# Optimization experiments

Hardware: AMD Instinct MI355X
Metric: run time of the kernel (lower is better)

The kernel has to match this reference:

```python
import jax, jax.numpy as jnp
import numpy as np

B, S, HID = 2, 2048, 1024
H, KVH = 16, 4           # query heads, kv heads
D = HID // H             # head_dim = 64
G = H // KVH             # group size (n_rep) = 4


def setup_inputs() -> dict:
    key = jax.random.key(0)
    ks = jax.random.split(key, 6)
    x = jax.random.normal(ks[0], (B, S, HID), dtype=jnp.float32)
    # RoPE tables: [S, D], standard theta=10000
    inv_freq = 1.0 / (10000.0 ** (jnp.arange(0, D, 2, dtype=jnp.float32) / D))
    freqs = jnp.arange(S, dtype=jnp.float32)[:, None] * inv_freq[None, :]  # [S, D/2]
    emb = jnp.concatenate([freqs, freqs], axis=-1)  # [S, D]
    cos, sin = jnp.cos(emb), jnp.sin(emb)
    scale = 0.02
    wq = jax.random.normal(ks[1], (HID, H * D), dtype=jnp.float32) * scale
    wk = jax.random.normal(ks[2], (HID, KVH * D), dtype=jnp.float32) * scale
    wv = jax.random.normal(ks[3], (HID, KVH * D), dtype=jnp.float32) * scale
    wo = jax.random.normal(ks[4], (H * D, HID), dtype=jnp.float32) * scale
    return {"x": x, "cos": cos, "sin": sin, "wq": wq, "wk": wk, "wv": wv, "wo": wo}


def _rotate_half(t):
    h = t.shape[-1] // 2
    return jnp.concatenate([-t[..., h:], t[..., :h]], axis=-1)


def reference(x, cos, sin, wq, wk, wv, wo):
    b, s, _ = x.shape
    q = (x @ wq).reshape(b, s, H, D)
    k = (x @ wk).reshape(b, s, KVH, D)
    v = (x @ wv).reshape(b, s, KVH, D)
    # RoPE (cos/sin broadcast over heads, unsqueeze_dim=1 -> [S,1,D])
    c = cos[:s, None, :]
    sn = sin[:s, None, :]
    q = q * c + _rotate_half(q) * sn
    k = k * c + _rotate_half(k) * sn
    # GQA attention without materializing repeated K/V: group q heads by kv head
    qg = q.reshape(b, s, KVH, G, D)
    scores = jnp.einsum('bqkgd,bskd->bkgqs', qg, k) / jnp.sqrt(jnp.asarray(D, q.dtype))
    causal = jnp.tril(jnp.ones((s, s), dtype=bool))  # [S_q, S_k]
    scores = jnp.where(causal[None, None, None, :, :], scores, -jnp.inf)
    p = jax.nn.softmax(scores, axis=-1)
    out = jnp.einsum('bkgqs,bskd->bqkgd', p, v).reshape(b, s, H * D)
    return out @ wo
```

## Files before the change

### kernel.cpp

```cpp
#include <hip/hip_runtime.h>
#include <hip/hip_bf16.h>


typedef short bfx4 __attribute__((ext_vector_type(4)));
typedef short bfx8 __attribute__((ext_vector_type(8)));
typedef float fx4  __attribute__((ext_vector_type(4)));
typedef float fx16 __attribute__((ext_vector_type(16)));
typedef unsigned int ux4 __attribute__((ext_vector_type(4)));

#define DEV __device__ __forceinline__
#define ALPHA 0.18033688011112042f

DEV void load_lds16(const void* g, void* l) {
  __builtin_amdgcn_global_load_lds(
      (const __attribute__((address_space(1))) unsigned int*)g,
      (__attribute__((address_space(3))) unsigned int*)l, 16, 0, 0);
}

DEV unsigned short f2bf(float f) {
  unsigned int x = __builtin_bit_cast(unsigned int, f);
  unsigned int r = (x + 0x7fffu + ((x >> 16) & 1u)) >> 16;
  return (unsigned short)r;
}
DEV float exp2_fast(float x) { float r; asm("v_exp_f32 %0, %1" : "=v"(r) : "v"(x)); return r; }
DEV unsigned cvtpk(float lo, float hi) {
  unsigned r; asm("v_cvt_pk_bf16_f32 %0, %1, %2" : "=v"(r) : "v"(lo), "v"(hi)); return r;
}
#define MFMA32 __builtin_amdgcn_mfma_f32_32x32x16_bf16


__global__ __launch_bounds__(256) void cvt_x_kernel(const float* __restrict__ x,
                                                    unsigned short* __restrict__ out) {
  int i = (blockIdx.x * 256 + threadIdx.x) * 8;
  fx4 a = *(const fx4*)(x + i);
  fx4 b = *(const fx4*)(x + i + 4);
  bfx8 r;
  r[0] = (short)f2bf(a[0]); r[1] = (short)f2bf(a[1]);
  r[2] = (short)f2bf(a[2]); r[3] = (short)f2bf(a[3]);
  r[4] = (short)f2bf(b[0]); r[5] = (short)f2bf(b[1]);
  r[6] = (short)f2bf(b[2]); r[7] = (short)f2bf(b[3]);
  *(bfx8*)(out + i) = r;
}


__global__ __launch_bounds__(256) void tw_kernel(const float* __restrict__ wq,
                                                 const float* __restrict__ wk,
                                                 const float* __restrict__ wv,
                                                 const float* __restrict__ wo,
                                                 unsigned short* __restrict__ wqkvT,
                                                 unsigned short* __restrict__ woT) {
  __shared__ float tile[64 * 65];
  const int bx = blockIdx.x;
  const int c0 = blockIdx.y * 64;
  const float* src; int ncols, rofs, r0; unsigned short* dst;
  if (bx < 24) {
    r0 = bx * 64; dst = wqkvT;
    if (r0 < 1024)      { src = wq; ncols = 1024; rofs = r0; }
    else if (r0 < 1280) { src = wk; ncols = 256;  rofs = r0 - 1024; }
    else                { src = wv; ncols = 256;  rofs = r0 - 1280; }
  } else {
    r0 = (bx - 24) * 64; dst = woT; src = wo; ncols = 1024; rofs = r0;
  }
  const int t = threadIdx.x;
#pragma unroll
  for (int p = 0; p < 4; ++p) {
    int idx = p * 256 + t;
    int cc = idx >> 4, q4 = idx & 15;
    fx4 v = *(const fx4*)(src + (size_t)(c0 + cc) * ncols + rofs + q4 * 4);
#pragma unroll
    for (int i = 0; i < 4; ++i) tile[(q4 * 4 + i) * 65 + cc] = v[i];
  }
  __syncthreads();
#pragma unroll
  for (int p = 0; p < 2; ++p) {
    int idx = p * 256 + t;
    int rr = idx >> 3, c8 = idx & 7;
    bfx8 v8;
#pragma unroll
    for (int i = 0; i < 8; ++i) v8[i] = (short)f2bf(tile[rr * 65 + c8 * 8 + i]);
    *(bfx8*)(dst + (size_t)(r0 + rr) * 1024 + c0 + c8 * 8) = v8;
  }
}


template <bool OUT_BF16, bool FUSE_ROPE>
__global__ __launch_bounds__(256) void gemm_bt_kernel(const unsigned short* __restrict__ A,
                                                      const unsigned short* __restrict__ Bt,
                                                      void* __restrict__ Cp,
                                                      int K, int ldc,
                                                      const float* __restrict__ ct,
                                                      const float* __restrict__ st,
                                                      unsigned short* __restrict__ vTout) {
  __shared__ __align__(16) unsigned short As[64 * 32];
  __shared__ __align__(16) unsigned short Bs[128 * 32];
  const int t = threadIdx.x;
  const int l = t & 63;
  const int w = t >> 6;
  const int wm = (w >> 1) * 32, wn = (w & 1) * 64;
  const int bm = blockIdx.x, bn = blockIdx.y;
  fx4 acc[2][4] = {};

  for (int kt = 0; kt < K; kt += 32) {
    __syncthreads();
    {
      int rr = t >> 2, ca = t & 3;
      int gca = ((ca ^ ((rr >> 1) & 3)) * 8);
      load_lds16(A + (size_t)(bm * 64 + rr) * K + kt + gca, (char*)As + t * 16);
    }
#pragma unroll
    for (int p = 0; p < 2; ++p) {
      int idx = p * 256 + t;
      int rr = idx >> 2, ca = idx & 3;
      int gca = ((ca ^ ((rr >> 1) & 3)) * 8);
      load_lds16(Bt + (size_t)(bn * 128 + rr) * K + kt + gca, (char*)Bs + idx * 16);
    }
    __syncthreads();

    bfx8 af[2], bfr[4];
#pragma unroll
    for (int mi = 0; mi < 2; ++mi) {
      int row = wm + mi * 16 + (l & 15);
      int ch = (l >> 4) ^ ((row >> 1) & 3);
      af[mi] = *(const bfx8*)(As + row * 32 + ch * 8);
    }
#pragma unroll
    for (int ni = 0; ni < 4; ++ni) {
      int rowb = wn + ni * 16 + (l & 15);
      int chb = (l >> 4) ^ ((rowb >> 1) & 3);
      bfr[ni] = *(const bfx8*)(Bs + rowb * 32 + chb * 8);
    }
#pragma unroll
    for (int mi = 0; mi < 2; ++mi)
#pragma unroll
      for (int ni = 0; ni < 4; ++ni)
        acc[mi][ni] = __builtin_amdgcn_mfma_f32_16x16x32_bf16(af[mi], bfr[ni], acc[mi][ni], 0, 0, 0);
  }

  const int colbase = bn * 128 + wn;
  if (FUSE_ROPE && colbase < 1280) {
    const float qsc = (colbase < 1024) ? ALPHA : 1.0f;
    unsigned short* Cb = (unsigned short*)Cp;
#pragma unroll
    for (int mi = 0; mi < 2; ++mi) {
      int row0 = bm * 64 + wm + mi * 16 + (l >> 4) * 4;
#pragma unroll
      for (int r = 0; r < 4; ++r) {
        int row = row0 + r, s = row & 2047;
#pragma unroll
        for (int ni = 0; ni < 2; ++ni) {
          int d = ni * 16 + (l & 15);
          float c = ct[s * 64 + d], sn = st[s * 64 + d];
          float x0 = acc[mi][ni][r], x1 = acc[mi][ni + 2][r];
          Cb[(size_t)row * 1280 + colbase + d]      = f2bf((x0 * c - x1 * sn) * qsc);
          Cb[(size_t)row * 1280 + colbase + d + 32] = f2bf((x1 * c + x0 * sn) * qsc);
        }
      }
    }
  } else if (FUSE_ROPE) {
    const int b4 = (bm >> 5) * 4;
#pragma unroll
    for (int mi = 0; mi < 2; ++mi) {
      int row0 = bm * 64 + wm + mi * 16 + (l >> 4) * 4;
      int s0r = row0 & 2047;
#pragma unroll
      for (int ni = 0; ni < 4; ++ni) {
        int vcol = colbase + ni * 16 + (l & 15) - 1280;
        int kvh = vcol >> 6, d = vcol & 63;
        bfx4 pv;
#pragma unroll
        for (int r = 0; r < 4; ++r) pv[r] = (short)f2bf(acc[mi][ni][r]);
        *(bfx4*)(vTout + ((size_t)(b4 + kvh) * 64 + d) * 2048 + s0r) = pv;
      }
    }
  } else {
#pragma unroll
    for (int mi = 0; mi < 2; ++mi) {
      int row0 = bm * 64 + wm + mi * 16 + (l >> 4) * 4;
#pragma unroll
      for (int ni = 0; ni < 4; ++ni) {
        int col = colbase + ni * 16 + (l & 15);
#pragma unroll
        for (int r = 0; r < 4; ++r) {
          if (OUT_BF16)
            ((unsigned short*)Cp)[(size_t)(row0 + r) * ldc + col] = f2bf(acc[mi][ni][r]);
          else
            ((float*)Cp)[(size_t)(row0 + r) * ldc + col] = acc[mi][ni][r];
        }
      }
    }
  }
}


__global__ __launch_bounds__(64, 2) void attn_kernel(const unsigned short* __restrict__ qkv,
                                                     const unsigned short* __restrict__ vT,
                                                     unsigned short* __restrict__ out) {
  __shared__ unsigned Ost[32 * 33];
  const int fid = blockIdx.x;
  const int Tp = 63 - (fid >> 5);
  const int hb = fid & 31;
  const int head = hb & 15, b = hb >> 4;
  const int kvh = head >> 2;
  const int l = threadIdx.x, q5 = l & 31, h = l >> 5;
  const int q0 = Tp * 32;
  const int nkb = (Tp >> 1) + 1;
  const size_t bbase = (size_t)b * 2048;
  const unsigned short* base = qkv + bbase * 1280;
  const unsigned short* kptr = base + 1024 + kvh * 64 + (size_t)q5 * 1280 + 8 * h;
  const unsigned short* vptr = vT + ((size_t)(b * 4 + kvh) * 64 + q5) * 2048 + 8 * h;

  bfx8 qf[4];
#pragma unroll
  for (int dd = 0; dd < 4; ++dd)
    qf[dd] = *(const bfx8*)(base + (size_t)(q0 + q5) * 1280 + head * 64 + dd * 16 + 8 * h);

  fx16 o[2] = {};
  float mrun = -1e30f, lrun = 0.f;
  bfx8 kfA[8], kfB[8], va[8];

#define LOADK(KF, KB) do {                                                       \
    const unsigned short* kq = kptr + (size_t)((KB) * 64) * 1280;                \
    KF[0] = *(const bfx8*)(kq);                                                  \
    KF[1] = *(const bfx8*)(kq + 16);                                             \
    KF[2] = *(const bfx8*)(kq + 32);                                             \
    KF[3] = *(const bfx8*)(kq + 48);                                             \
    const unsigned short* kq1 = kq + 32 * 1280;                                  \
    KF[4] = *(const bfx8*)(kq1);                                                 \
    KF[5] = *(const bfx8*)(kq1 + 16);                                            \
    KF[6] = *(const bfx8*)(kq1 + 32);                                            \
    KF[7] = *(const bfx8*)(kq1 + 48);                                            \
  } while (0)

#define LOADV(KB) do {                                                           \
    const unsigned short* vq = vptr + (KB) * 64;                                 \
    va[0] = *(const bfx8*)(vq);                                                  \
    va[1] = *(const bfx8*)(vq + 16);                                             \
    va[2] = *(const bfx8*)(vq + 32);                                             \
    va[3] = *(const bfx8*)(vq + 48);                                             \
    const unsigned short* vq1 = vq + 32 * 2048;                                  \
    va[4] = *(const bfx8*)(vq1);                                                 \
    va[5] = *(const bfx8*)(vq1 + 16);                                            \
    va[6] = *(const bfx8*)(vq1 + 32);                                            \
    va[7] = *(const bfx8*)(vq1 + 48);                                            \
  } while (0)

#define STEP(KF, KB) do {                                                        \
    fx16 s0 = {}, s1 = {};                                                       \
    __builtin_amdgcn_s_setprio(1);                                               \
    s0 = MFMA32(KF[0], qf[0], s0, 0, 0, 0);                                      \
    s1 = MFMA32(KF[4], qf[0], s1, 0, 0, 0);                                      \
    s0 = MFMA32(KF[1], qf[1], s0, 0, 0, 0);                                      \
    s1 = MFMA32(KF[5], qf[1], s1, 0, 0, 0);                                      \
    s0 = MFMA32(KF[2], qf[2], s0, 0, 0, 0);                                      \
    s1 = MFMA32(KF[6], qf[2], s1, 0, 0, 0);                                      \
    s0 = MFMA32(KF[3], qf[3], s0, 0, 0, 0);                                      \
    s1 = MFMA32(KF[7], qf[3], s1, 0, 0, 0);                                      \
    __builtin_amdgcn_s_setprio(0);                                               \
    if ((KB) == nkb - 1) {                                                       \
      const int j0s = (KB) * 64;                                                 \
      _Pragma("unroll")                                                          \
      for (int r = 0; r < 16; ++r) {                                             \
        int key0 = j0s + (r & 3) + 8 * (r >> 2) + 4 * h;                         \
        if (key0 > q0 + q5) s0[r] = -1e30f;                                      \
        if (key0 + 32 > q0 + q5) s1[r] = -1e30f;                                 \
      }                                                                          \
    }                                                                            \
    float pmax = fmaxf(s0[0], s1[0]);                                            \
    _Pragma("unroll")                                                            \
    for (int r = 1; r < 16; ++r) pmax = fmaxf(pmax, fmaxf(s0[r], s1[r]));        \
    pmax = fmaxf(pmax, __shfl_xor(pmax, 32, 64));                                \
    if (!__all(pmax <= mrun + 8.0f)) {                                           \
      float mnew = fmaxf(mrun, pmax);                                            \
      float corr = exp2_fast(mrun - mnew);                                       \
      mrun = mnew;                                                               \
      lrun *= corr;                                                              \
      o[0] *= corr; o[1] *= corr;                                                \
    }                                                                            \
    float lt0 = 0.f, lt1 = 0.f;                                                  \
    _Pragma("unroll")                                                            \
    for (int r = 0; r < 16; ++r) {                                               \
      float p0 = exp2_fast(s0[r] - mrun); s0[r] = p0; lt0 += p0;                 \
      float p1 = exp2_fast(s1[r] - mrun); s1[r] = p1; lt1 += p1;                 \
    }                                                                            \
    float lt = lt0 + lt1;                                                        \
    lt += __shfl_xor(lt, 32, 64);                                                \
    lrun += lt;                                                                  \
    unsigned U[2][8];                                                            \
    _Pragma("unroll")                                                            \
    for (int k8 = 0; k8 < 8; ++k8) {                                             \
      U[0][k8] = cvtpk(s0[2 * k8], s0[2 * k8 + 1]);                              \
      U[1][k8] = cvtpk(s1[2 * k8], s1[2 * k8 + 1]);                              \
    }                                                                            \
    _Pragma("unroll")                                                            \
    for (int hs = 0; hs < 2; ++hs) {                                             \
      _Pragma("unroll")                                                          \
      for (int e = 0; e < 2; ++e) {                                              \
        unsigned send0 = h ? U[hs][4 * e] : U[hs][4 * e + 2];                    \
        unsigned send1 = h ? U[hs][4 * e + 1] : U[hs][4 * e + 3];                \
        unsigned r0 = (unsigned)__shfl_xor((int)send0, 32, 64);                  \
        unsigned r1 = (unsigned)__shfl_xor((int)send1, 32, 64);                  \
        unsigned k0 = h ? U[hs][4 * e + 2] : U[hs][4 * e];                       \
        unsigned k1 = h ? U[hs][4 * e + 3] : U[hs][4 * e + 1];                   \
        ux4 fr;                                                                  \
        fr[0] = h ? r0 : k0; fr[1] = h ? r1 : k1;                                \
        fr[2] = h ? k0 : r0; fr[3] = h ? k1 : r1;                                \
        bfx8 pf = __builtin_bit_cast(bfx8, fr);                                  \
        __builtin_amdgcn_s_setprio(1);                                           \
        o[0] = MFMA32(va[2 * hs + e], pf, o[0], 0, 0, 0);                        \
        o[1] = MFMA32(va[4 + 2 * hs + e], pf, o[1], 0, 0, 0);                    \
        __builtin_amdgcn_s_setprio(0);                                           \
      }                                                                          \
    }                                                                            \
  } while (0)

  LOADK(kfA, 0);
  int kb = 0;
  while (true) {
    LOADV(kb);
    if (kb + 1 < nkb) LOADK(kfB, kb + 1);
    STEP(kfA, kb);
    ++kb; if (kb >= nkb) break;
    LOADV(kb);
    if (kb + 1 < nkb) LOADK(kfA, kb + 1);
    STEP(kfB, kb);
    ++kb; if (kb >= nkb) break;
  }
#undef LOADK
#undef LOADV
#undef STEP

  float inv = 1.0f / lrun;
#pragma unroll
  for (int dt = 0; dt < 2; ++dt)
#pragma unroll
    for (int rp = 0; rp < 8; ++rp) {
      int r = 2 * rp;
      int d = 32 * dt + (r & 3) + 8 * (r >> 2) + 4 * h;
      Ost[q5 * 33 + (d >> 1)] = cvtpk(o[dt][r] * inv, o[dt][r + 1] * inv);
    }
  asm volatile("s_waitcnt lgkmcnt(0)" ::: "memory");
  __builtin_amdgcn_sched_barrier(0);
  {
    int rr = l >> 1, half = l & 1;
    const unsigned* src = Ost + rr * 33 + half * 16;
    unsigned short* dst = out + (bbase + q0 + rr) * 1024 + head * 64 + half * 32;
#pragma unroll
    for (int u2 = 0; u2 < 4; ++u2) {
      ux4 v4;
      v4[0] = src[4 * u2]; v4[1] = src[4 * u2 + 1];
      v4[2] = src[4 * u2 + 2]; v4[3] = src[4 * u2 + 3];
      *(ux4*)(dst + u2 * 8) = v4;
    }
  }
}


extern "C" void kernel_launch(void* const* d_in, const int* in_sizes, int n_in,
                              void* d_out, int out_size, void* d_ws, size_t ws_size,
                              hipStream_t stream) {
  const float* x    = (const float*)d_in[0];
  const float* cosb = (const float*)d_in[1];
  const float* sinb = (const float*)d_in[2];
  const float* wq   = (const float*)d_in[3];
  const float* wk   = (const float*)d_in[4];
  const float* wv   = (const float*)d_in[5];
  const float* wo   = (const float*)d_in[6];
  float* out = (float*)d_out;

  char* ws = (char*)d_ws;
  unsigned short* xb    = (unsigned short*)ws;
  unsigned short* attn  = (unsigned short*)ws;
  unsigned short* wqkvT = (unsigned short*)(ws + 8388608);
  unsigned short* woT   = (unsigned short*)(ws + 11534336);
  unsigned short* qkv   = (unsigned short*)(ws + 13631488);
  unsigned short* vT    = (unsigned short*)(ws + 24117248);

  cvt_x_kernel<<<2048, 256, 0, stream>>>(x, xb);
  tw_kernel<<<dim3(40, 16), 256, 0, stream>>>(wq, wk, wv, wo, wqkvT, woT);
  gemm_bt_kernel<true, true><<<dim3(64, 12), 256, 0, stream>>>(xb, wqkvT, qkv, 1024, 1280, cosb, sinb, vT);
  attn_kernel<<<2048, 64, 0, stream>>>(qkv, vT, attn);
  gemm_bt_kernel<false, false><<<dim3(64, 8), 256, 0, stream>>>(attn, woT, out, 1024, 1024, nullptr, nullptr, nullptr);
}
```

Measured before the change: 203.6 us.

## Share K/V tiles in LDS across four waves with double-buffered async staging

The attention kernel moves from one 64-thread wave per 32-query tile to 256-thread blocks of four waves covering 128 queries. The waves share K and V tiles that are staged into swizzled LDS with double-buffered global_load_lds. Previously each wave loaded its own K/V fragments straight from global memory into registers. The change cuts redundant global traffic and register pressure. In exchange it adds block-wide barriers and LDS reads, and waves with shorter causal ranges sit idle at the barriers. It also reorders the tile schedule so heavy and light blocks are interleaved.

```diff
diff --git a/kernel.cpp b/kernel.cpp
--- a/kernel.cpp
+++ b/kernel.cpp
@@ -192,22 +192,28 @@
 }
 
 
-__global__ __launch_bounds__(64, 2) void attn_kernel(const unsigned short* __restrict__ qkv,
-                                                     const unsigned short* __restrict__ vT,
-                                                     unsigned short* __restrict__ out) {
-  __shared__ unsigned Ost[32 * 33];
-  const int fid = blockIdx.x;
-  const int Tp = 63 - (fid >> 5);
-  const int hb = fid & 31;
+__global__ __launch_bounds__(256, 2) void attn_kernel(const unsigned short* __restrict__ qkv,
+                                                      const unsigned short* __restrict__ vT,
+                                                      unsigned short* __restrict__ out) {
+  __shared__ __align__(16) unsigned short Kl[2][64 * 64];
+  __shared__ __align__(16) unsigned short Vl[2][64 * 64];
+  __shared__ unsigned Ost[4][32 * 33];
+
+  const int bx = blockIdx.x;
+  const int g = bx >> 5;
+  const int T = (g < 8) ? (15 - g) : (g - 8);
+  const int hb = bx & 31;
   const int head = hb & 15, b = hb >> 4;
   const int kvh = head >> 2;
-  const int l = threadIdx.x, q5 = l & 31, h = l >> 5;
-  const int q0 = Tp * 32;
-  const int nkb = (Tp >> 1) + 1;
+  const int t = threadIdx.x, w = t >> 6, l = t & 63;
+  const int q5 = l & 31, h = l >> 5;
+  const int q0 = T * 128 + w * 32;
+  const int nkb = 2 * T + 2;
+  const int kbd = 2 * T + (w >> 1);
   const size_t bbase = (size_t)b * 2048;
   const unsigned short* base = qkv + bbase * 1280;
-  const unsigned short* kptr = base + 1024 + kvh * 64 + (size_t)q5 * 1280 + 8 * h;
-  const unsigned short* vptr = vT + ((size_t)(b * 4 + kvh) * 64 + q5) * 2048 + 8 * h;
+  const unsigned short* kbase = base + 1024 + kvh * 64;
+  const unsigned short* vbase = vT + (size_t)(b * 4 + kvh) * 64 * 2048;
 
   bfx8 qf[4];
 #pragma unroll
@@ -216,47 +222,47 @@
 
   fx16 o[2] = {};
   float mrun = -1e30f, lrun = 0.f;
-  bfx8 kfA[8], kfB[8], va[8];
-
-#define LOADK(KF, KB) do {                                                       \
-    const unsigned short* kq = kptr + (size_t)((KB) * 64) * 1280;                \
-    KF[0] = *(const bfx8*)(kq);                                                  \
-    KF[1] = *(const bfx8*)(kq + 16);                                             \
-    KF[2] = *(const bfx8*)(kq + 32);                                             \
-    KF[3] = *(const bfx8*)(kq + 48);                                             \
-    const unsigned short* kq1 = kq + 32 * 1280;                                  \
-    KF[4] = *(const bfx8*)(kq1);                                                 \
-    KF[5] = *(const bfx8*)(kq1 + 16);                                            \
-    KF[6] = *(const bfx8*)(kq1 + 32);                                            \
-    KF[7] = *(const bfx8*)(kq1 + 48);                                            \
+
+#define STAGE(NXT, KBN) do {                                                     \
+    const int j0n = (KBN) * 64;                                                  \
+    _Pragma("unroll")                                                            \
+    for (int p = 0; p < 2; ++p) {                                                \
+      int idx = p * 256 + t, j = idx >> 3, c = idx & 7;                          \
+      int gc = (c ^ (j & 7)) * 8;                                                \
+      load_lds16(kbase + (size_t)(j0n + j) * 1280 + gc,                          \
+                 (char*)&Kl[NXT][0] + idx * 16);                                 \
+    }                                                                            \
+    _Pragma("unroll")                                                            \
+    for (int p = 0; p < 2; ++p) {                                                \
+      int idx = p * 256 + t, j = idx >> 3, c = idx & 7;                          \
+      int gc = (c ^ (j & 7)) * 8;                                                \
+      load_lds16(vbase + (size_t)j * 2048 + j0n + gc,                            \
+                 (char*)&Vl[NXT][0] + idx * 16);                                 \
+    }                                                                            \
   } while (0)
 
-#define LOADV(KB) do {                                                           \
-    const unsigned short* vq = vptr + (KB) * 64;                                 \
-    va[0] = *(const bfx8*)(vq);                                                  \
-    va[1] = *(const bfx8*)(vq + 16);                                             \
-    va[2] = *(const bfx8*)(vq + 32);                                             \
-    va[3] = *(const bfx8*)(vq + 48);                                             \
-    const unsigned short* vq1 = vq + 32 * 2048;                                  \
-    va[4] = *(const bfx8*)(vq1);                                                 \
-    va[5] = *(const bfx8*)(vq1 + 16);                                            \
-    va[6] = *(const bfx8*)(vq1 + 32);                                            \
-    va[7] = *(const bfx8*)(vq1 + 48);                                            \
-  } while (0)
-
-#define STEP(KF, KB) do {                                                        \
+#define STEP(CUR, KB) do {                                                       \
+    const char* Kb = (const char*)&Kl[CUR][0];                                   \
+    const char* Vb = (const char*)&Vl[CUR][0];                                   \
+    bfx8 kf0[4], kf1[4];                                                         \
+    _Pragma("unroll")                                                            \
+    for (int dd = 0; dd < 4; ++dd) {                                             \
+      int slot = ((2 * dd + h) ^ (q5 & 7)) * 16;                                 \
+      kf0[dd] = *(const bfx8*)(Kb + q5 * 128 + slot);                            \
+      kf1[dd] = *(const bfx8*)(Kb + (32 + q5) * 128 + slot);                     \
+    }                                                                            \
     fx16 s0 = {}, s1 = {};                                                       \
     __builtin_amdgcn_s_setprio(1);                                               \
-    s0 = MFMA32(KF[0], qf[0], s0, 0, 0, 0);                                      \
-    s1 = MFMA32(KF[4], qf[0], s1, 0, 0, 0);                                      \
-    s0 = MFMA32(KF[1], qf[1], s0, 0, 0, 0);                                      \
-    s1 = MFMA32(KF[5], qf[1], s1, 0, 0, 0);                                      \
-    s0 = MFMA32(KF[2], qf[2], s0, 0, 0, 0);                                      \
-    s1 = MFMA32(KF[6], qf[2], s1, 0, 0, 0);                                      \
-    s0 = MFMA32(KF[3], qf[3], s0, 0, 0, 0);                                      \
-    s1 = MFMA32(KF[7], qf[3], s1, 0, 0, 0);                                      \
+    s0 = MFMA32(kf0[0], qf[0], s0, 0, 0, 0);                                     \
+    s1 = MFMA32(kf1[0], qf[0], s1, 0, 0, 0);                                     \
+    s0 = MFMA32(kf0[1], qf[1], s0, 0, 0, 0);                                     \
+    s1 = MFMA32(kf1[1], qf[1], s1, 0, 0, 0);                                     \
+    s0 = MFMA32(kf0[2], qf[2], s0, 0, 0, 0);                                     \
+    s1 = MFMA32(kf1[2], qf[2], s1, 0, 0, 0);                                     \
+    s0 = MFMA32(kf0[3], qf[3], s0, 0, 0, 0);                                     \
+    s1 = MFMA32(kf1[3], qf[3], s1, 0, 0, 0);                                     \
     __builtin_amdgcn_s_setprio(0);                                               \
-    if ((KB) == nkb - 1) {                                                       \
+    if ((KB) == kbd) {                                                           \
       const int j0s = (KB) * 64;                                                 \
       _Pragma("unroll")                                                          \
       for (int r = 0; r < 16; ++r) {                                             \
@@ -305,44 +311,45 @@
         fr[0] = h ? r0 : k0; fr[1] = h ? r1 : k1;                                \
         fr[2] = h ? k0 : r0; fr[3] = h ? k1 : r1;                                \
         bfx8 pf = __builtin_bit_cast(bfx8, fr);                                  \
+        int ks = 2 * hs + e;                                                     \
+        int vslot = ((2 * ks + h) ^ (q5 & 7)) * 16;                              \
+        bfx8 vf0 = *(const bfx8*)(Vb + q5 * 128 + vslot);                        \
+        bfx8 vf1 = *(const bfx8*)(Vb + (32 + q5) * 128 + vslot);                 \
         __builtin_amdgcn_s_setprio(1);                                           \
-        o[0] = MFMA32(va[2 * hs + e], pf, o[0], 0, 0, 0);                        \
-        o[1] = MFMA32(va[4 + 2 * hs + e], pf, o[1], 0, 0, 0);                    \
+        o[0] = MFMA32(vf0, pf, o[0], 0, 0, 0);                                   \
+        o[1] = MFMA32(vf1, pf, o[1], 0, 0, 0);                                   \
         __builtin_amdgcn_s_setprio(0);                                           \
       }                                                                          \
     }                                                                            \
   } while (0)
 
-  LOADK(kfA, 0);
-  int kb = 0;
-  while (true) {
-    LOADV(kb);
-    if (kb + 1 < nkb) LOADK(kfB, kb + 1);
-    STEP(kfA, kb);
-    ++kb; if (kb >= nkb) break;
-    LOADV(kb);
-    if (kb + 1 < nkb) LOADK(kfA, kb + 1);
-    STEP(kfB, kb);
-    ++kb; if (kb >= nkb) break;
-  }
-#undef LOADK
-#undef LOADV
+  STAGE(0, 0);
+  __syncthreads();
+#pragma unroll 1
+  for (int kb = 0; kb < nkb; ++kb) {
+    const int cur = kb & 1;
+    if (kb + 1 < nkb) STAGE(cur ^ 1, kb + 1);
+    if (kb <= kbd) STEP(cur, kb);
+    __syncthreads();
+  }
+#undef STAGE
 #undef STEP
 
   float inv = 1.0f / lrun;
+  unsigned* OstW = &Ost[w][0];
 #pragma unroll
   for (int dt = 0; dt < 2; ++dt)
 #pragma unroll
     for (int rp = 0; rp < 8; ++rp) {
       int r = 2 * rp;
       int d = 32 * dt + (r & 3) + 8 * (r >> 2) + 4 * h;
-      Ost[q5 * 33 + (d >> 1)] = cvtpk(o[dt][r] * inv, o[dt][r + 1] * inv);
+      OstW[q5 * 33 + (d >> 1)] = cvtpk(o[dt][r] * inv, o[dt][r + 1] * inv);
     }
   asm volatile("s_waitcnt lgkmcnt(0)" ::: "memory");
   __builtin_amdgcn_sched_barrier(0);
   {
     int rr = l >> 1, half = l & 1;
-    const unsigned* src = Ost + rr * 33 + half * 16;
+    const unsigned* src = OstW + rr * 33 + half * 16;
     unsigned short* dst = out + (bbase + q0 + rr) * 1024 + head * 64 + half * 32;
 #pragma unroll
     for (int u2 = 0; u2 < 4; ++u2) {
@@ -378,6 +385,6 @@
   cvt_x_kernel<<<2048, 256, 0, stream>>>(x, xb);
   tw_kernel<<<dim3(40, 16), 256, 0, stream>>>(wq, wk, wv, wo, wqkvT, woT);
   gemm_bt_kernel<true, true><<<dim3(64, 12), 256, 0, stream>>>(xb, wqkvT, qkv, 1024, 1280, cosb, sinb, vT);
-  attn_kernel<<<2048, 64, 0, stream>>>(qkv, vT, attn);
+  attn_kernel<<<512, 256, 0, stream>>>(qkv, vT, attn);
   gemm_bt_kernel<false, false><<<dim3(64, 8), 256, 0, stream>>>(attn, woT, out, 1024, 1024, nullptr, nullptr, nullptr);
 }
```

Measured after the change: 183.8 us. 1.11x faster.
